# Kernel optimization log

Measured on AMD Instinct MI355X. Metric: run time of the kernel, lower is better.

The kernel has to match this reference:

```python
import jax, jax.numpy as jnp
import numpy as np

B, G, S, GS, P = 32, 512, 128, 32, 10
C, H, RED = 384, 6, 16
HID = 4 * C
D = C // H
SCALE = D ** -0.5

def _gelu(x):
    return jax.nn.gelu(x, approximate=False)

def _ln(x, g, b):
    m = jnp.mean(x, -1, keepdims=True)
    v = jnp.var(x, -1, keepdims=True)
    return (x - m) * jax.lax.rsqrt(v + 1e-5) * g + b

def _split_qkv(x, W):
    Bn, T, Cc = x.shape
    qkv = (x @ W).reshape(Bn, T, 3, H, D).transpose(2, 0, 3, 1, 4)
    return qkv[0], qkv[1], qkv[2]

def _merge(x):
    Bn, Hh, T, Dd = x.shape
    return x.transpose(0, 2, 1, 3).reshape(Bn, T, Hh * Dd)

def _mha(q, k, v):
    a = jax.nn.softmax(jnp.einsum('bhnd,bhmd->bhnm', q, k) * SCALE, axis=-1)
    return jnp.einsum('bhnm,bhmd->bhnd', a, v)

def _forward(x, center1, center2, neighborhood, prompt_embeddings, ln1_g, ln1_b, Wqkv, Wproj, bproj, gate, ln2_g, ln2_b, W1, b1, W2, b2, ad_down_W, ad_down_b, ad_up_W, ad_up_b, ad_gate, bn_g, bn_b, bn_mean, bn_var, ln3_g, ln3_b, a1_Wqkv, a1_Wproj, a1_bproj, ad1_down_W, ad1_down_b, ad1_up_W, ad1_up_b, idx, center_idx, group_size, if_maxmean, pro_cof, center_cof):
    Bx, Ntok, Cc = x.shape
    # prompt dropout is identity in eval
    prompt = jnp.broadcast_to(prompt_embeddings, (Bx, P, Cc))
    # --- gated dual self / prompt-cross attention ---
    xn = _ln(x, ln1_g, ln1_b)
    q, k, v = _split_qkv(xn, Wqkv)
    xs = _mha(q, k, v)                                  # [B,H,N,D]
    _, pk, pv = _split_qkv(prompt, Wqkv)
    pa = jax.nn.softmax(jnp.einsum('bhnd,bhpd->bhnp', q, pk) * SCALE, axis=-1)
    px = jnp.einsum('bhnp,bhpd->bhnd', gate * pa, pv)   # learned gate per head
    x = x + (_merge(xs) + _merge(px)) @ Wproj + bproj
    # --- MLP + gated bottleneck adapter residual ---
    h = _gelu(_ln(x, ln2_g, ln2_b) @ W1 + b1) @ W2 + b2
    h_ad = h + _gelu(h @ ad_down_W + ad_down_b) @ ad_up_W + ad_up_b
    x = ad_gate * h_ad + x
    cls_x = x[:, :1]
    xt = x[:, 1:]                                       # [B,G,C]
    flat = xt.reshape(Bx * G, Cc)
    x_nb = flat[idx].reshape(Bx * S, group_size, Cc)    # KNN neighborhoods
    x_ct = flat[center_idx].reshape(Bx, S, Cc)          # center features
    # NOTE: original normalizes `neighborhood` by its std, but result is unused
    # --- local self-attention (attn1 over norm3) on each neighborhood ---
    nq, nk, nv = _split_qkv(_ln(x_nb, ln3_g, ln3_b), a1_Wqkv)
    no = _mha(nq, nk, nv)
    x_nb = x_nb + _merge(no) @ a1_Wproj + a1_bproj
    knn = x_nb.reshape(Bx, S, group_size, Cc)
    lc = jnp.max(knn, axis=2)
    if if_maxmean:
        lc = lc + jnp.mean(knn, axis=2)
    # BatchNorm1d (eval, running stats) + GELU over channel dim
    lc = _gelu((lc - bn_mean) * jax.lax.rsqrt(bn_var + 1e-5) * bn_g + bn_b)
    vis = lc + center_cof * x_ct                        # [B,S,C]
    # --- propagate: de_neighbors == S so sorted-topk == full weighted sum ---
    d = jnp.sum((center1[:, :, None, :] - center2[:, None, :, :]) ** 2, axis=-1)  # [B,G,S]
    w = 1.0 / (d + 1e-8)
    w = w / jnp.sum(w, axis=-1, keepdims=True)
    interp = jnp.einsum('bns,bsc->bnc', w, vis)
    xt = xt + pro_cof * interp
    out = jnp.concatenate([cls_x, xt], axis=1)
    # adapter1
    out = out + _gelu(out @ ad1_down_W + ad1_down_b) @ ad1_up_W + ad1_up_b
    return out

def setup_inputs():
    ks = jax.random.split(jax.random.key(0), 20)
    r = lambda i, shape, s=0.02: jax.random.normal(ks[i], shape, jnp.float32) * s
    return {
        'x': jax.random.normal(ks[0], (B, G + 1, C), jnp.float32),
        'center1': jax.random.normal(ks[1], (B, G, 3), jnp.float32),
        'center2': jax.random.normal(ks[2], (B, S, 3), jnp.float32),
        'neighborhood': jax.random.normal(ks[3], (B, S, GS, 3), jnp.float32),
        'prompt_embeddings': r(4, (P, C)),
        'ln1_g': jnp.ones(C), 'ln1_b': jnp.zeros(C),
        'Wqkv': r(5, (C, 3 * C)),
        'Wproj': r(6, (C, C)), 'bproj': jnp.zeros(C),
        'gate': jax.random.normal(ks[7], (1, H, 1, 1), jnp.float32),
        'ln2_g': jnp.ones(C), 'ln2_b': jnp.zeros(C),
        'W1': r(8, (C, HID)), 'b1': jnp.zeros(HID),
        'W2': r(9, (HID, C)), 'b2': jnp.zeros(C),
        'ad_down_W': r(10, (C, RED)), 'ad_down_b': jnp.zeros(RED),
        'ad_up_W': r(11, (RED, C)), 'ad_up_b': jnp.zeros(C),
        'ad_gate': jax.random.normal(ks[12], (), jnp.float32),
        'bn_g': jnp.ones(C), 'bn_b': jnp.zeros(C),
        'bn_mean': jnp.zeros(C), 'bn_var': jnp.ones(C),
        'ln3_g': jnp.ones(C), 'ln3_b': jnp.zeros(C),
        'a1_Wqkv': r(13, (C, 3 * C)),
        'a1_Wproj': r(14, (C, C)), 'a1_bproj': jnp.zeros(C),
        'ad1_down_W': r(15, (C, RED)), 'ad1_down_b': jnp.zeros(RED),
        'ad1_up_W': r(16, (RED, C)), 'ad1_up_b': jnp.zeros(C),
        'idx': jax.random.randint(ks[17], (B * S * GS,), 0, B * G),
        'center_idx': jax.random.randint(ks[18], (B * S,), 0, B * G),
        'group_size': GS,
        'if_maxmean': 1,
        'pro_cof': 1,
        'center_cof': 1,
    }

def reference(x, center1, center2, neighborhood, prompt_embeddings, ln1_g, ln1_b, Wqkv, Wproj, bproj, gate, ln2_g, ln2_b, W1, b1, W2, b2, ad_down_W, ad_down_b, ad_up_W, ad_up_b, ad_gate, bn_g, bn_b, bn_mean, bn_var, ln3_g, ln3_b, a1_Wqkv, a1_Wproj, a1_bproj, ad1_down_W, ad1_down_b, ad1_up_W, ad1_up_b, idx, center_idx, group_size, if_maxmean, pro_cof, center_cof):
    return _forward(x, center1, center2, neighborhood, prompt_embeddings, ln1_g, ln1_b, Wqkv, Wproj, bproj, gate, ln2_g, ln2_b, W1, b1, W2, b2, ad_down_W, ad_down_b, ad_up_W, ad_up_b, ad_gate, bn_g, bn_b, bn_mean, bn_var, ln3_g, ln3_b, a1_Wqkv, a1_Wproj, a1_bproj, ad1_down_W, ad1_down_b, ad1_up_W, ad1_up_b, idx, center_idx, group_size, if_maxmean, pro_cof, center_cof)
```

## Files before the change

### kernel.cpp

```cpp
#include <hip/hip_runtime.h>
#include <hip/hip_bf16.h>
#include <cstdint>
#include <cstddef>

typedef __hip_bfloat16 bf16;
constexpr int TOK = 32 * 513;

typedef __attribute__((ext_vector_type(8))) short short8;
typedef __attribute__((ext_vector_type(4))) float f32x4;

__device__ __forceinline__ float bflo(unsigned u){ return __uint_as_float(u << 16); }
__device__ __forceinline__ float bfhi(unsigned u){ return __uint_as_float(u & 0xffff0000u); }
__device__ __forceinline__ float b2f(bf16 x){ return __bfloat162float(x); }
__device__ __forceinline__ bf16  f2b(float x){ return __float2bfloat16(x); }
__device__ __forceinline__ float geluf(float x){ return 0.5f*x*(1.0f + erff(x*0.70710678118654752f)); }
__device__ __forceinline__ void unp8(uint4 u, float* f){
  f[0]=bflo(u.x); f[1]=bfhi(u.x); f[2]=bflo(u.y); f[3]=bfhi(u.y);
  f[4]=bflo(u.z); f[5]=bfhi(u.z); f[6]=bflo(u.w); f[7]=bfhi(u.w);
}
__device__ __forceinline__ float scal(const int* p){
  const int i = *p;
  if (i > -1000000 && i < 1000000) return (float)i;
  return __int_as_float(i);
}
__device__ __forceinline__ f32x4 mfma16(short8 a, short8 b, f32x4 c){
  return __builtin_amdgcn_mfma_f32_16x16x32_bf16(a, b, c, 0, 0, 0);
}
__device__ __forceinline__ int swzl(int l){ return l ^ ((l >> 3) & 7); }

__global__ __launch_bounds__(256) void detect_kernel(const unsigned* __restrict__ x,
                                                     int* __restrict__ flag)
{
  const int t = threadIdx.x;
  bool bad = false;
  for (int i = t; i < 2048; i += 256){
    const unsigned u = x[i];
    const float a = fabsf(bflo(u)), b = fabsf(bfhi(u));
    if (!(a < 1e6f) || !(b < 1e6f)) bad = true;
  }
  __shared__ int s;
  if (t == 0) s = 0;
  __syncthreads();
  const unsigned long long m = __ballot(bad);
  if (m != 0ull && (t & 63) == 0) atomicOr(&s, 1);
  __syncthreads();
  if (t == 0) *flag = s;
}

struct ConvArgs {
  const void* src[34];
  bf16*       dst[34];
  int         n[34];
};
__global__ __launch_bounds__(256) void convert_many(const int* __restrict__ flag, ConvArgs a)
{
  const int ii = blockIdx.y;
  const bool isf = (*flag != 0);
  const int n = a.n[ii];
  const int n8 = n >> 3;
  bf16* d = a.dst[ii];
  if (isf){
    const float4* s = (const float4*)a.src[ii];
    for (int i = blockIdx.x*256 + threadIdx.x; i < n8; i += gridDim.x*256){
      const float4 f0 = s[i*2];
      const float4 f1 = s[i*2 + 1];
      bf16 tmp[8] = {f2b(f0.x),f2b(f0.y),f2b(f0.z),f2b(f0.w),
                     f2b(f1.x),f2b(f1.y),f2b(f1.z),f2b(f1.w)};
      *(uint4*)(d + (size_t)i*8) = *(const uint4*)tmp;
    }
  } else {
    const uint4* s = (const uint4*)a.src[ii];
    for (int i = blockIdx.x*256 + threadIdx.x; i < n8; i += gridDim.x*256){
      ((uint4*)d)[i] = s[i];
    }
  }
  if (blockIdx.x == 0){
    for (int i = n8*8 + threadIdx.x; i < n; i += 256){
      d[i] = isf ? f2b(((const float*)a.src[ii])[i]) : ((const bf16*)a.src[ii])[i];
    }
  }
}

__global__ __launch_bounds__(256) void shuffle_b(const bf16* __restrict__ W,
    bf16* __restrict__ out, int N, int KT, int NT)
{
  const int id = blockIdx.x*256 + threadIdx.x;
  if (id >= NT*KT*64) return;
  const int l  = id & 63;
  const int k0 = (id >> 6) % KT;
  const int n0 = (id >> 6) / KT;
  bf16 tmp[8];
  #pragma unroll
  for (int j = 0; j < 8; j++)
    tmp[j] = W[(size_t)(k0*32 + (l>>4)*8 + j)*N + n0*16 + (l&15)];
  *(uint4*)(out + (size_t)id*8) = *(const uint4*)tmp;
}

template<bool SRC_BF16>
__global__ __launch_bounds__(256) void ln_kernel(const void* __restrict__ src,
    const bf16* __restrict__ g, const bf16* __restrict__ b,
    bf16* __restrict__ out, int rows)
{
  const int wave = (blockIdx.x * blockDim.x + threadIdx.x) >> 6;
  const int lane = threadIdx.x & 63;
  if (wave >= rows) return;
  float v[6]; float s = 0.f, s2 = 0.f;
  #pragma unroll
  for (int i = 0; i < 6; i++){
    const int c = lane + 64*i;
    float x;
    if (SRC_BF16) x = b2f(((const bf16*)src)[(size_t)wave*384 + c]);
    else          x = ((const float*)src)[(size_t)wave*384 + c];
    v[i] = x; s += x; s2 += x*x;
  }
  #pragma unroll
  for (int mm = 32; mm; mm >>= 1){ s += __shfl_xor(s, mm); s2 += __shfl_xor(s2, mm); }
  const float mean = s * (1.f/384.f);
  const float rs = rsqrtf(s2 * (1.f/384.f) - mean*mean + 1e-5f);
  #pragma unroll
  for (int i = 0; i < 6; i++){
    const int c = lane + 64*i;
    out[(size_t)wave*384 + c] = f2b((v[i]-mean)*rs*b2f(g[c]) + b2f(b[c]));
  }
}

__global__ __launch_bounds__(256) void ln3_kernel(const float* __restrict__ xres,
    const bf16* __restrict__ g, const bf16* __restrict__ b, bf16* __restrict__ out)
{
  const int r = (blockIdx.x * blockDim.x + threadIdx.x) >> 6;
  const int lane = threadIdx.x & 63;
  if (r >= 16384) return;
  const int tok = (r >> 9)*513 + 1 + (r & 511);
  const float* xp = xres + (size_t)tok*384;
  float v[6]; float s = 0.f, s2 = 0.f;
  #pragma unroll
  for (int i = 0; i < 6; i++){
    const float x = xp[lane + 64*i];
    v[i] = x; s += x; s2 += x*x;
  }
  #pragma unroll
  for (int mm = 32; mm; mm >>= 1){ s += __shfl_xor(s, mm); s2 += __shfl_xor(s2, mm); }
  const float mean = s * (1.f/384.f);
  const float rs = rsqrtf(s2 * (1.f/384.f) - mean*mean + 1e-5f);
  #pragma unroll
  for (int i = 0; i < 6; i++){
    const int c = lane + 64*i;
    out[(size_t)r*384 + c] = f2b((v[i]-mean)*rs*b2f(g[c]) + b2f(b[c]));
  }
}

template<int EPI>
__global__ __launch_bounds__(256) void mfma_gemm(
    const bf16* __restrict__ A, const bf16* __restrict__ Bsh,
    const bf16* __restrict__ bias, const bf16* __restrict__ resid,
    void* __restrict__ outv, int M, int N, int K)
{
  __shared__ __align__(16) bf16 sA[8*64*8];
  const int t = threadIdx.x, lane = t & 63, w = t >> 6;
  const int l15 = lane & 15, quad = lane >> 4;
  const int wm = w & 1, wn = w >> 1;
  const int m0 = blockIdx.y * 128;
  const int n0t = blockIdx.x * 8 + wn * 4;
  const int KT = K >> 5;
  f32x4 acc[4][4];
  #pragma unroll
  for (int i = 0; i < 4; i++){
    #pragma unroll
    for (int j = 0; j < 4; j++) acc[i][j] = f32x4{0.f,0.f,0.f,0.f};
  }
  const int arow = t >> 1, ac0 = (t & 1) * 16;
  const int amt = arow >> 4, al15 = arow & 15, aq0 = (ac0 >> 3);

  for (int ks = 0; ks < KT; ks++){
    uint4 u0 = {0,0,0,0}, u1 = {0,0,0,0};
    const int gm = m0 + arow;
    if (gm < M){
      const bf16* ap = A + (size_t)gm*K + ks*32 + ac0;
      u0 = *(const uint4*)ap; u1 = *(const uint4*)(ap + 8);
    }
    *(uint4*)(sA + ((amt*64 + aq0*16     + al15) << 3)) = u0;
    *(uint4*)(sA + ((amt*64 + (aq0+1)*16 + al15) << 3)) = u1;
    __syncthreads();
    short8 afr[4];
    #pragma unroll
    for (int i = 0; i < 4; i++)
      afr[i] = *(const short8*)(sA + (((wm*4+i)*64 + lane) << 3));
    #pragma unroll
    for (int j = 0; j < 4; j++){
      const short8 b = *(const short8*)(Bsh + ((size_t)((n0t+j)*KT + ks)*64 + lane)*8);
      #pragma unroll
      for (int i = 0; i < 4; i++) acc[i][j] = mfma16(afr[i], b, acc[i][j]);
    }
    __syncthreads();
  }
  #pragma unroll
  for (int i = 0; i < 4; i++){
    #pragma unroll
    for (int r = 0; r < 4; r++){
      const int gm = m0 + (wm*4+i)*16 + quad*4 + r;
      if (gm < M){
        #pragma unroll
        for (int j = 0; j < 4; j++){
          const int gn = (n0t+j)*16 + l15;
          float v = acc[i][j][r];
          const size_t o = (size_t)gm*N + gn;
          if (EPI == 0){ v += b2f(bias[gn]); ((bf16*)outv)[o] = f2b(v); }
          else if (EPI == 1){ ((bf16*)outv)[o] = f2b(v); }
          else if (EPI == 2){ v += b2f(bias[gn]); ((bf16*)outv)[o] = f2b(geluf(v)); }
          else { v += b2f(bias[gn]) + b2f(resid[o]); ((float*)outv)[o] = v; }
        }
      }
    }
  }
}

__global__ __launch_bounds__(256) void pqkv_kernel(const bf16* __restrict__ pe,
    const bf16* __restrict__ Wqkv, float* __restrict__ pq)
{
  const int n  = blockIdx.x*64 + (threadIdx.x & 63);
  const int rg = threadIdx.x >> 6;
  for (int r = rg; r < 10; r += 4){
    float s0 = 0.f, s1 = 0.f;
    for (int c = 0; c < 384; c += 2){
      s0 = fmaf(b2f(pe[(size_t)r*384+c]),   b2f(Wqkv[(size_t)c*1152 + n]),     s0);
      s1 = fmaf(b2f(pe[(size_t)r*384+c+1]), b2f(Wqkv[(size_t)(c+1)*1152 + n]), s1);
    }
    pq[(size_t)r*1152 + n] = s0 + s1;
  }
}

__global__ __launch_bounds__(256) void attn_kernel(
    const bf16* __restrict__ qkv, const float* __restrict__ pq,
    const bf16* __restrict__ gate, bf16* __restrict__ ao)
{
  __shared__ __align__(16) bf16 s_q[64*72];
  __shared__ __align__(16) bf16 s_k[64*72];
  __shared__ __align__(16) bf16 s_vT[64*72];
  __shared__ __align__(16) bf16 s_p[4*16*40];
  __shared__ __align__(16) bf16 s_pk[16*72];
  __shared__ __align__(16) bf16 s_pvT[64*40];
  const int bh = blockIdx.y;
  const int b = bh / 6, h = bh % 6;
  const int q0 = blockIdx.x * 64;
  const int t = threadIdx.x, lane = t & 63, w = t >> 6;
  const int l15 = lane & 15, quad = lane >> 4;

  {
    const int row = t >> 2, dc = (t & 3) * 16;
    const int tok = q0 + row;
    uint4 u0 = {0,0,0,0}, u1 = {0,0,0,0};
    if (tok < 513){
      const bf16* p = qkv + (size_t)(b*513 + tok)*1152 + h*64 + dc;
      u0 = *(const uint4*)p; u1 = *(const uint4*)(p + 8);
    }
    *(uint4*)(s_q + row*72 + dc)     = u0;
    *(uint4*)(s_q + row*72 + dc + 8) = u1;
  }
  {
    const int j = t >> 4, dc = (t & 15) * 4;
    float f[4] = {0.f,0.f,0.f,0.f};
    if (j < 10){
      const float* pk = pq + (size_t)j*1152 + 384 + h*64 + dc;
      f[0]=pk[0]; f[1]=pk[1]; f[2]=pk[2]; f[3]=pk[3];
    }
    bf16 tmp[4] = {f2b(f[0]),f2b(f[1]),f2b(f[2]),f2b(f[3])};
    *(uint2*)(s_pk + j*72 + dc) = *(const uint2*)tmp;
  }
  {
    const int d = t & 63, kg = t >> 6;
    #pragma unroll
    for (int kk = 0; kk < 8; kk++){
      const int key = kg*8 + kk;
      bf16 v = f2b(0.f);
      if (key < 10) v = f2b(pq[(size_t)key*1152 + 768 + h*64 + d]);
      s_pvT[d*40 + key] = v;
    }
  }

  float m_i[4], l_i[4];
  f32x4 oacc[4];
  #pragma unroll
  for (int r = 0; r < 4; r++){ m_i[r] = -30000.f; l_i[r] = 0.f; }
  #pragma unroll
  for (int nt = 0; nt < 4; nt++) oacc[nt] = f32x4{0.f,0.f,0.f,0.f};
  bf16* myp = s_p + w*16*40;
  const short8* aq = (const short8*)(s_q + (w*16 + l15)*72);

  for (int kt = 0; kt < 9; kt++){
    const int kb = kt*64;
    __syncthreads();
    {
      const int kp = t & 31, dg = t >> 5;
      const int key0 = kb + 2*kp;
      uint4 k0v = {0,0,0,0}, k1v = {0,0,0,0}, v0 = {0,0,0,0}, v1 = {0,0,0,0};
      if (key0 < 513){
        const bf16* base = qkv + (size_t)(b*513 + key0)*1152 + h*64 + dg*8;
        k0v = *(const uint4*)(base + 384);
        v0  = *(const uint4*)(base + 768);
      }
      if (key0 + 1 < 513){
        const bf16* base = qkv + (size_t)(b*513 + key0 + 1)*1152 + h*64 + dg*8;
        k1v = *(const uint4*)(base + 384);
        v1  = *(const uint4*)(base + 768);
      }
      *(uint4*)(s_k + (2*kp)*72   + dg*8) = k0v;
      *(uint4*)(s_k + (2*kp+1)*72 + dg*8) = k1v;
      const unsigned short* a0 = (const unsigned short*)&v0;
      const unsigned short* a1 = (const unsigned short*)&v1;
      unsigned* vt = (unsigned*)s_vT;
      #pragma unroll
      for (int j = 0; j < 8; j++)
        vt[(dg*8 + j)*36 + kp] = (unsigned)a0[j] | ((unsigned)a1[j] << 16);
    }
    __syncthreads();

    f32x4 sreg[4];
    #pragma unroll
    for (int nt = 0; nt < 4; nt++){
      f32x4 acc = f32x4{0.f,0.f,0.f,0.f};
      const short8* bk = (const short8*)(s_k + (nt*16 + l15)*72);
      acc = mfma16(aq[quad],     bk[quad],     acc);
      acc = mfma16(aq[4 + quad], bk[4 + quad], acc);
      const bool kvalid = (kb + nt*16 + l15) < 513;
      #pragma unroll
      for (int r = 0; r < 4; r++)
        sreg[nt][r] = kvalid ? acc[r]*0.125f : -30000.f;
    }
    float alpha[4];
    #pragma unroll
    for (int r = 0; r < 4; r++){
      float mx = fmaxf(fmaxf(sreg[0][r], sreg[1][r]), fmaxf(sreg[2][r], sreg[3][r]));
      #pragma unroll
      for (int mm = 8; mm; mm >>= 1) mx = fmaxf(mx, __shfl_xor(mx, mm));
      const float mn = fmaxf(m_i[r], mx);
      alpha[r] = __expf(m_i[r] - mn);
      m_i[r] = mn;
      float ps = 0.f;
      #pragma unroll
      for (int nt = 0; nt < 4; nt++){
        const float p = __expf(sreg[nt][r] - mn);
        sreg[nt][r] = p; ps += p;
      }
      #pragma unroll
      for (int mm = 8; mm; mm >>= 1) ps += __shfl_xor(ps, mm);
      l_i[r] = l_i[r]*alpha[r] + ps;
    }
    #pragma unroll
    for (int nt = 0; nt < 4; nt++){
      #pragma unroll
      for (int r = 0; r < 4; r++)
        myp[(quad*4 + r)*40 + nt*16 + l15] = f2b(sreg[nt][r]);
    }
    #pragma unroll
    for (int nt = 0; nt < 4; nt++){
      #pragma unroll
      for (int r = 0; r < 4; r++) oacc[nt][r] *= alpha[r];
    }
    const short8* ap = (const short8*)(myp + l15*40);
    #pragma unroll
    for (int nt = 0; nt < 4; nt++){
      const short8* bv = (const short8*)(s_vT + (nt*16 + l15)*72);
      oacc[nt] = mfma16(ap[quad],     bv[quad],     oacc[nt]);
      oacc[nt] = mfma16(ap[4 + quad], bv[4 + quad], oacc[nt]);
    }
  }

  f32x4 sp;
  {
    f32x4 acc = f32x4{0.f,0.f,0.f,0.f};
    const short8* bp = (const short8*)(s_pk + l15*72);
    acc = mfma16(aq[quad],     bp[quad],     acc);
    acc = mfma16(aq[4 + quad], bp[4 + quad], acc);
    #pragma unroll
    for (int r = 0; r < 4; r++)
      sp[r] = (l15 < 10) ? acc[r]*0.125f : -30000.f;
  }
  float psr[4];
  #pragma unroll
  for (int r = 0; r < 4; r++){
    float mx = sp[r];
    #pragma unroll
    for (int mm = 8; mm; mm >>= 1) mx = fmaxf(mx, __shfl_xor(mx, mm));
    const float p = __expf(sp[r] - mx);
    float ps = p;
    #pragma unroll
    for (int mm = 8; mm; mm >>= 1) ps += __shfl_xor(ps, mm);
    psr[r] = ps;
    myp[(quad*4 + r)*40 + l15]      = f2b(p);
    myp[(quad*4 + r)*40 + 16 + l15] = f2b(0.f);
  }
  f32x4 pva[4];
  {
    const short8* ap = (const short8*)(myp + l15*40);
    #pragma unroll
    for (int nt = 0; nt < 4; nt++){
      const short8* bv = (const short8*)(s_pvT + (nt*16 + l15)*40);
      pva[nt] = mfma16(ap[quad], bv[quad], f32x4{0.f,0.f,0.f,0.f});
    }
  }

  const float gh = b2f(gate[h]);
  #pragma unroll
  for (int r = 0; r < 4; r++){
    const int tok = q0 + w*16 + quad*4 + r;
    if (tok < 513){
      const float invl = 1.f/l_i[r];
      const float gps  = gh/psr[r];
      #pragma unroll
      for (int nt = 0; nt < 4; nt++){
        const float val = oacc[nt][r]*invl + pva[nt][r]*gps;
        ao[(size_t)(b*513 + tok)*384 + h*64 + nt*16 + l15] = f2b(val);
      }
    }
  }
}

__global__ __launch_bounds__(256) void adapter_mid_kernel(const bf16* __restrict__ h,
    const bf16* __restrict__ Wd, const bf16* __restrict__ bd,
    const bf16* __restrict__ Wu, const bf16* __restrict__ bu,
    const bf16* __restrict__ p_gate, float* __restrict__ xres)
{
  __shared__ float s_h[384];
  __shared__ float s_part[16][17];
  __shared__ float s_y[16];
  const size_t row = blockIdx.x;
  const int t = threadIdx.x;
  const bf16* hp = h + row*384;
  for (int c = t; c < 384; c += 256) s_h[c] = b2f(hp[c]);
  __syncthreads();
  const int o = t & 15, p = t >> 4;
  float part0 = 0.f, part1 = 0.f;
  for (int c = p; c < 384; c += 32){
    part0 = fmaf(s_h[c],    b2f(Wd[(size_t)c*16 + o]),      part0);
    part1 = fmaf(s_h[c+16], b2f(Wd[(size_t)(c+16)*16 + o]), part1);
  }
  s_part[o][p] = part0 + part1;
  __syncthreads();
  if (t < 16){
    float sum = 0.f;
    #pragma unroll
    for (int pp = 0; pp < 16; pp++) sum += s_part[t][pp];
    s_y[t] = geluf(sum + b2f(bd[t]));
  }
  __syncthreads();
  const float g = b2f(p_gate[0]);
  for (int c = t; c < 384; c += 256){
    float up = 0.f;
    #pragma unroll
    for (int o2 = 0; o2 < 16; o2++) up = fmaf(s_y[o2], b2f(Wu[(size_t)o2*384 + c]), up);
    const float had = s_h[c] + up + b2f(bu[c]);
    xres[row*384 + c] = g*had + xres[row*384 + c];
  }
}

__global__ __launch_bounds__(256) void adapter_final_kernel(const float* __restrict__ xr,
    const bf16* __restrict__ Wd, const bf16* __restrict__ bd,
    const bf16* __restrict__ Wu, const bf16* __restrict__ bu,
    const int* __restrict__ flag, void* __restrict__ out)
{
  __shared__ float s_h[384];
  __shared__ float s_part[16][17];
  __shared__ float s_y[16];
  const size_t row = blockIdx.x;
  const int t = threadIdx.x;
  const float* hp = xr + row*384;
  for (int c = t; c < 384; c += 256) s_h[c] = hp[c];
  __syncthreads();
  const int o = t & 15, p = t >> 4;
  float part0 = 0.f, part1 = 0.f;
  for (int c = p; c < 384; c += 32){
    part0 = fmaf(s_h[c],    b2f(Wd[(size_t)c*16 + o]),      part0);
    part1 = fmaf(s_h[c+16], b2f(Wd[(size_t)(c+16)*16 + o]), part1);
  }
  s_part[o][p] = part0 + part1;
  __syncthreads();
  if (t < 16){
    float sum = 0.f;
    #pragma unroll
    for (int pp = 0; pp < 16; pp++) sum += s_part[t][pp];
    s_y[t] = geluf(sum + b2f(bd[t]));
  }
  __syncthreads();
  const bool isf = (*flag != 0);
  for (int c = t; c < 384; c += 256){
    float up = 0.f;
    #pragma unroll
    for (int o2 = 0; o2 < 16; o2++) up = fmaf(s_y[o2], b2f(Wu[(size_t)o2*384 + c]), up);
    const float v = s_h[c] + up + b2f(bu[c]);
    if (isf) ((float*)out)[row*384 + c] = v;
    else     ((bf16*)out)[row*384 + c] = f2b(v);
  }
}

__global__ __launch_bounds__(512) void local_kernel(
    const bf16* __restrict__ qkv3, const float* __restrict__ xres,
    const int* __restrict__ idx, const int* __restrict__ cidx,
    const bf16* __restrict__ Bp, const bf16* __restrict__ bp1,
    const bf16* __restrict__ bng, const bf16* __restrict__ bnb,
    const bf16* __restrict__ bnm, const bf16* __restrict__ bnv,
    const int* __restrict__ p_ifmm, const int* __restrict__ p_ccof,
    float* __restrict__ vis)
{
  __shared__ __align__(16) bf16 sQ[3*4*64*8];
  __shared__ __align__(16) bf16 sK[3*4*64*8];
  __shared__ __align__(16) bf16 sV[3*4*64*8];
  __shared__ __align__(16) bf16 sP[3*2*64*8];
  __shared__ int s_flat[32];
  __shared__ int s_tok[32];
  bf16* sO = sQ;

  const int g = blockIdx.x;
  const int t = threadIdx.x, lane = t & 63, w = t >> 6;
  const int l15 = lane & 15, quad = lane >> 4;
  const int lanez = swzl(lane);

  if (t < 32){
    const int r = idx[g*32 + t];
    s_flat[t] = r;
    s_tok[t]  = (r >> 9)*513 + 1 + (r & 511);
  }
  __syncthreads();

  f32x4 accp[3][2];
  #pragma unroll
  for (int a = 0; a < 3; a++){
    #pragma unroll
    for (int m = 0; m < 2; m++) accp[a][m] = f32x4{0.f,0.f,0.f,0.f};
  }

  for (int hc = 0; hc < 2; hc++){
    for (int ch = t; ch < 2304; ch += 512){
      const int row = ch & 31;
      const int cc  = ch >> 5;
      const int seg = cc / 24;
      const int wi  = cc - seg*24;
      const int h   = wi >> 3;
      const int d0  = (wi & 7) * 8;
      const int col = seg*384 + (hc*3 + h)*64 + d0;
      const uint4 u = *(const uint4*)(qkv3 + (size_t)s_flat[row]*1152 + col);
      if (seg < 2){
        const int T = h*4 + (row>>4)*2 + (d0>>5);
        const int L = ((d0>>3)&3)*16 + (row&15);
        const int addr = (T*64 + swzl(L))*8;
        if (seg == 0) *(uint4*)(sQ + addr) = u;
        else          *(uint4*)(sK + addr) = u;
      } else {
        const bf16* sv = (const bf16*)&u;
        #pragma unroll
        for (int j2 = 0; j2 < 8; j2++){
          const int d = d0 + j2;
          const int L = (row>>3)*16 + (d&15);
          sV[((h*4 + (d>>4))*64 + swzl(L))*8 + (row&7)] = sv[j2];
        }
      }
    }
    __syncthreads();

    if (w < 6){
      const int h = w >> 1, mt = w & 1;
      f32x4 sr[2];
      #pragma unroll
      for (int nt = 0; nt < 2; nt++){
        f32x4 acc = f32x4{0.f,0.f,0.f,0.f};
        #pragma unroll
        for (int k0 = 0; k0 < 2; k0++){
          const short8 a = *(const short8*)(sQ + ((h*4 + mt*2 + k0)*64 + lanez)*8);
          const short8 b = *(const short8*)(sK + ((h*4 + nt*2 + k0)*64 + lanez)*8);
          acc = mfma16(a, b, acc);
        }
        #pragma unroll
        for (int r = 0; r < 4; r++) sr[nt][r] = acc[r]*0.125f;
      }
      #pragma unroll
      for (int r = 0; r < 4; r++){
        float mx = fmaxf(sr[0][r], sr[1][r]);
        #pragma unroll
        for (int mm = 8; mm; mm >>= 1) mx = fmaxf(mx, __shfl_xor(mx, mm));
        const float e0 = __expf(sr[0][r] - mx), e1 = __expf(sr[1][r] - mx);
        float sm = e0 + e1;
        #pragma unroll
        for (int mm = 8; mm; mm >>= 1) sm += __shfl_xor(sm, mm);
        const float inv = 1.f/sm;
        const int m = quad*4 + r;
        const int L0 = (l15 >> 3)*16       + m;
        const int L1 = (2 + (l15 >> 3))*16 + m;
        sP[((h*2 + mt)*64 + swzl(L0))*8 + (l15 & 7)] = f2b(e0*inv);
        sP[((h*2 + mt)*64 + swzl(L1))*8 + (l15 & 7)] = f2b(e1*inv);
      }
    }
    __syncthreads();

    {
      const int mt = w & 1, nt = w >> 1;
      const int k0w = nt >> 1, qdw = (nt & 1)*2 + (l15 >> 3), jw = l15 & 7;
      #pragma unroll
      for (int h = 0; h < 3; h++){
        const short8 a = *(const short8*)(sP + ((h*2 + mt)*64 + lanez)*8);
        const short8 b = *(const short8*)(sV + ((h*4 + nt)*64 + lanez)*8);
        const f32x4 o = mfma16(a, b, f32x4{0.f,0.f,0.f,0.f});
        #pragma unroll
        for (int r = 0; r < 4; r++){
          const int L = qdw*16 + quad*4 + r;
          sO[((h*4 + mt*2 + k0w)*64 + swzl(L))*8 + jw] = f2b(o[r]);
        }
      }
    }
    __syncthreads();

    #pragma unroll
    for (int h = 0; h < 3; h++){
      short8 afr[2][2];
      #pragma unroll
      for (int mt = 0; mt < 2; mt++){
        #pragma unroll
        for (int k0l = 0; k0l < 2; k0l++)
          afr[mt][k0l] = *(const short8*)(sO + ((h*4 + mt*2 + k0l)*64 + lanez)*8);
      }
      const int hg2 = (hc*3 + h)*2;
      #pragma unroll
      for (int tt = 0; tt < 3; tt++){
        const int nt = w*3 + tt;
        #pragma unroll
        for (int k0l = 0; k0l < 2; k0l++){
          const short8 b = *(const short8*)(Bp + ((size_t)(nt*12 + hg2 + k0l)*64 + lane)*8);
          accp[tt][0] = mfma16(afr[0][k0l], b, accp[tt][0]);
          accp[tt][1] = mfma16(afr[1][k0l], b, accp[tt][1]);
        }
      }
    }
    __syncthreads();
  }

  const float fmm  = scal(p_ifmm);
  const float ccof = scal(p_ccof);
  const int cr = cidx[g];
  const int ctok = (cr >> 9)*513 + 1 + (cr & 511);
  #pragma unroll
  for (int tt = 0; tt < 3; tt++){
    const int n = (w*3 + tt)*16 + l15;
    const float bb = b2f(bp1[n]);
    float mx = -3e30f, sm = 0.f;
    #pragma unroll
    for (int mt = 0; mt < 2; mt++){
      #pragma unroll
      for (int r = 0; r < 4; r++){
        const int tok = mt*16 + quad*4 + r;
        const float v = accp[tt][mt][r] + bb + xres[(size_t)s_tok[tok]*384 + n];
        mx = fmaxf(mx, v); sm += v;
      }
    }
    mx = fmaxf(mx, __shfl_xor(mx, 16)); sm += __shfl_xor(sm, 16);
    mx = fmaxf(mx, __shfl_xor(mx, 32)); sm += __shfl_xor(sm, 32);
    if (quad == 0){
      const float lc = (fmm != 0.f) ? (mx + sm*(1.f/32.f)) : mx;
      const float nr = (lc - b2f(bnm[n])) * rsqrtf(b2f(bnv[n]) + 1e-5f) * b2f(bng[n]) + b2f(bnb[n]);
      vis[(size_t)g*384 + n] = geluf(nr) + ccof * xres[(size_t)ctok*384 + n];
    }
  }
}

__global__ __launch_bounds__(256) void interp_kernel(const bf16* __restrict__ c1,
    const bf16* __restrict__ c2, const float* __restrict__ vis,
    const int* __restrict__ p_pcof, float* __restrict__ xres)
{
  __shared__ float s_w[8][128];
  __shared__ float s_red[2];
  const int b = blockIdx.y;
  const int n0 = blockIdx.x * 8;
  const int t = threadIdx.x;
  for (int ni = 0; ni < 8; ni++){
    const int n = n0 + ni;
    float wv = 0.f;
    if (t < 128){
      float d2 = 0.f;
      #pragma unroll
      for (int k = 0; k < 3; k++){
        const float a = b2f(c1[((size_t)b*512 + n)*3 + k]);
        const float c = b2f(c2[((size_t)b*128 + t)*3 + k]);
        const float df = a - c; d2 += df*df;
      }
      wv = 1.f/(d2 + 1e-8f);
    }
    float rsum = wv;
    #pragma unroll
    for (int mm = 32; mm; mm >>= 1) rsum += __shfl_xor(rsum, mm);
    if (((t & 63) == 0) && t < 128) s_red[t >> 6] = rsum;
    __syncthreads();
    const float tot = s_red[0] + s_red[1];
    if (t < 128) s_w[ni][t] = wv / tot;
    __syncthreads();
  }
  float acc1[8], acc2[8];
  #pragma unroll
  for (int ni = 0; ni < 8; ni++){ acc1[ni] = 0.f; acc2[ni] = 0.f; }
  for (int s = 0; s < 128; s++){
    const float* vp = vis + ((size_t)b*128 + s)*384;
    const float v1 = vp[t];
    const float v2 = (t < 128) ? vp[t + 256] : 0.f;
    #pragma unroll
    for (int ni = 0; ni < 8; ni++){
      const float wn = s_w[ni][s];
      acc1[ni] = fmaf(wn, v1, acc1[ni]);
      acc2[ni] = fmaf(wn, v2, acc2[ni]);
    }
  }
  const float pc = scal(p_pcof);
  #pragma unroll
  for (int ni = 0; ni < 8; ni++){
    const int tok = b*513 + 1 + n0 + ni;
    xres[(size_t)tok*384 + t] += pc*acc1[ni];
    if (t < 128) xres[(size_t)tok*384 + t + 256] += pc*acc2[ni];
  }
}

extern "C" void kernel_launch(void* const* d_in, const int* in_sizes, int n_in,
                              void* d_out, int out_size, void* d_ws, size_t ws_size,
                              hipStream_t stream)
{
  (void)n_in; (void)out_size; (void)ws_size;
  const int*  idx   = (const int*)d_in[35];
  const int*  cidx  = (const int*)d_in[36];
  const int*  ifmm  = (const int*)d_in[38];
  const int*  pcof  = (const int*)d_in[39];
  const int*  ccof  = (const int*)d_in[40];

  size_t off = 0;
  auto alloc = [&](size_t bytes) -> void* {
    void* p = (char*)d_ws + off; off += (bytes + 255) & ~(size_t)255; return p;
  };
  int*   flag = (int*)  alloc(sizeof(int));
  float* xres = (float*)alloc((size_t)TOK*384*4);
  bf16*  slab = (bf16*) alloc((size_t)TOK*1536*2);
  bf16*  xn   = (bf16*) alloc((size_t)TOK*384*2);
  float* pq   = (float*)alloc((size_t)10*1152*4);
  bf16*  Bq   = (bf16*) alloc((size_t)72*12*64*8*2);
  bf16*  Bp   = (bf16*) alloc((size_t)24*12*64*8*2);
  bf16*  Bqkv = (bf16*) alloc((size_t)72*12*64*8*2);
  bf16*  Bw1  = (bf16*) alloc((size_t)96*12*64*8*2);
  bf16*  Bw2  = (bf16*) alloc((size_t)24*48*64*8*2);
  bf16*  Bwp  = (bf16*) alloc((size_t)24*12*64*8*2);

  bf16*  qkvb = slab;
  bf16*  x_c  = slab + (size_t)TOK*1152;
  bf16*  h1   = slab;
  bf16*  qkv3 = slab;
  bf16*  xln3 = slab + (size_t)TOK*1152;
  bf16*  ao   = xn;
  bf16*  hbuf = xn;
  float* visb = (float*)xn;

  const int conv_ids[34] = {0,1,2,4,5,6,7,8,9,10,11,12,13,14,15,16,17,
                            18,19,20,21,22,23,24,25,26,27,28,29,30,31,32,33,34};
  ConvArgs ca;
  bf16* canon[41];
  int maxn = 1;
  for (int k = 0; k < 34; k++){
    const int i = conv_ids[k];
    const int n = in_sizes[i];
    bf16* dst = (i == 0) ? x_c : (bf16*)alloc((size_t)n*2);
    ca.src[k] = d_in[i]; ca.dst[k] = dst; ca.n[k] = n;
    canon[i] = dst;
    if (n > maxn) maxn = n;
  }
  detect_kernel<<<dim3(1), dim3(256), 0, stream>>>((const unsigned*)d_in[0], flag);
  {
    int gx = (maxn/8 + 255) / 256; if (gx > 512) gx = 512; if (gx < 1) gx = 1;
    convert_many<<<dim3(gx, 34), dim3(256), 0, stream>>>(flag, ca);
  }

  const bf16 *x_in = canon[0], *c1 = canon[1], *c2 = canon[2], *pe = canon[4],
             *ln1g = canon[5], *ln1b = canon[6], *Wqkv = canon[7], *Wproj = canon[8],
             *bproj = canon[9], *gate = canon[10], *ln2g = canon[11], *ln2b = canon[12],
             *W1 = canon[13], *b1 = canon[14], *W2 = canon[15], *b2v = canon[16],
             *adW = canon[17], *adb = canon[18], *adU = canon[19], *adub = canon[20],
             *adg = canon[21], *bng = canon[22], *bnb = canon[23], *bnm = canon[24],
             *bnv = canon[25], *ln3g = canon[26], *ln3b = canon[27], *a1W = canon[28],
             *a1P = canon[29], *a1pb = canon[30], *d1W = canon[31], *d1b = canon[32],
             *u1W = canon[33], *u1b = canon[34];

  shuffle_b<<<dim3(216), dim3(256), 0, stream>>>(a1W, Bq, 1152, 12, 72);
  shuffle_b<<<dim3(72),  dim3(256), 0, stream>>>(a1P, Bp, 384, 12, 24);
  shuffle_b<<<dim3(216), dim3(256), 0, stream>>>(Wqkv, Bqkv, 1152, 12, 72);
  shuffle_b<<<dim3(288), dim3(256), 0, stream>>>(W1, Bw1, 1536, 12, 96);
  shuffle_b<<<dim3(288), dim3(256), 0, stream>>>(W2, Bw2, 384, 48, 24);
  shuffle_b<<<dim3(72),  dim3(256), 0, stream>>>(Wproj, Bwp, 384, 12, 24);

  ln_kernel<true><<<dim3((TOK*64)/256), dim3(256), 0, stream>>>((const void*)x_in, ln1g, ln1b, xn, TOK);
  mfma_gemm<1><<<dim3(9,129), dim3(256), 0, stream>>>(xn, Bqkv, nullptr, nullptr, qkvb, TOK, 1152, 384);
  pqkv_kernel<<<dim3(18), dim3(256), 0, stream>>>(pe, Wqkv, pq);
  attn_kernel<<<dim3(9,192), dim3(256), 0, stream>>>(qkvb, pq, gate, ao);
  mfma_gemm<3><<<dim3(3,129), dim3(256), 0, stream>>>(ao, Bwp, bproj, x_in, xres, TOK, 384, 384);
  ln_kernel<false><<<dim3((TOK*64)/256), dim3(256), 0, stream>>>((const void*)xres, ln2g, ln2b, xn, TOK);
  mfma_gemm<2><<<dim3(12,129), dim3(256), 0, stream>>>(xn, Bw1, b1, nullptr, h1, TOK, 1536, 384);
  mfma_gemm<0><<<dim3(3,129), dim3(256), 0, stream>>>(h1, Bw2, b2v, nullptr, hbuf, TOK, 384, 1536);
  adapter_mid_kernel<<<dim3(TOK), dim3(256), 0, stream>>>(hbuf, adW, adb, adU, adub, adg, xres);
  ln3_kernel<<<dim3((16384*64)/256), dim3(256), 0, stream>>>(xres, ln3g, ln3b, xln3);
  mfma_gemm<1><<<dim3(9,128), dim3(256), 0, stream>>>(xln3, Bq, nullptr, nullptr, qkv3, 16384, 1152, 384);
  local_kernel<<<dim3(4096), dim3(512), 0, stream>>>(qkv3, xres, idx, cidx, Bp, a1pb,
                                                     bng, bnb, bnm, bnv, ifmm, ccof, visb);
  interp_kernel<<<dim3(64,32), dim3(256), 0, stream>>>(c1, c2, visb, pcof, xres);
  adapter_final_kernel<<<dim3(TOK), dim3(256), 0, stream>>>(xres, d1W, d1b, u1W, u1b, flag, d_out);
}
```

Before: 808.8 us.

## Load Q/K fragments directly from global and prefetch V into registers

The local attention kernel stops staging Q and K through shared memory and has each wave load its MFMA operand fragments straight from the gathered qkv rows in global memory. V for the next head chunk is prefetched into registers during the projection phase, and the head-chunk loop is unrolled. Launch bounds now request 8 waves per SIMD to push occupancy, with reduced LDS footprint. The cost is more scattered global loads, with K rows reread by several waves, and possible register pressure or spills under the tighter bound.

```diff
diff --git a/kernel.cpp b/kernel.cpp
--- a/kernel.cpp
+++ b/kernel.cpp
@@ -492,7 +492,7 @@
   }
 }
 
-__global__ __launch_bounds__(512) void local_kernel(
+__global__ __launch_bounds__(512, 8) void local_kernel(
     const bf16* __restrict__ qkv3, const float* __restrict__ xres,
     const int* __restrict__ idx, const int* __restrict__ cidx,
     const bf16* __restrict__ Bp, const bf16* __restrict__ bp1,
@@ -501,13 +501,11 @@
     const int* __restrict__ p_ifmm, const int* __restrict__ p_ccof,
     float* __restrict__ vis)
 {
-  __shared__ __align__(16) bf16 sQ[3*4*64*8];
-  __shared__ __align__(16) bf16 sK[3*4*64*8];
   __shared__ __align__(16) bf16 sV[3*4*64*8];
   __shared__ __align__(16) bf16 sP[3*2*64*8];
+  __shared__ __align__(16) bf16 sO[3*4*64*8];
   __shared__ int s_flat[32];
   __shared__ int s_tok[32];
-  bf16* sO = sQ;
 
   const int g = blockIdx.x;
   const int t = threadIdx.x, lane = t & 63, w = t >> 6;
@@ -521,6 +519,18 @@
   }
   __syncthreads();
 
+  const int vrowA = t & 31,          vccA = t >> 5;
+  const int vrowB = (512 + t) & 31,  vccB = (512 + t) >> 5;
+  const int vhA = vccA >> 3, vd0A = (vccA & 7) * 8;
+  const int vhB = vccB >> 3, vd0B = (vccB & 7) * 8;
+  const bool hasB = (t < 256);
+
+  uint4 svA, svB;
+  {
+    svA = *(const uint4*)(qkv3 + (size_t)s_flat[vrowA]*1152 + 768 + (0*3 + vhA)*64 + vd0A);
+    if (hasB) svB = *(const uint4*)(qkv3 + (size_t)s_flat[vrowB]*1152 + 768 + (0*3 + vhB)*64 + vd0B);
+  }
+
   f32x4 accp[3][2];
   #pragma unroll
   for (int a = 0; a < 3; a++){
@@ -528,29 +538,23 @@
     for (int m = 0; m < 2; m++) accp[a][m] = f32x4{0.f,0.f,0.f,0.f};
   }
 
+  #pragma unroll
   for (int hc = 0; hc < 2; hc++){
-    for (int ch = t; ch < 2304; ch += 512){
-      const int row = ch & 31;
-      const int cc  = ch >> 5;
-      const int seg = cc / 24;
-      const int wi  = cc - seg*24;
-      const int h   = wi >> 3;
-      const int d0  = (wi & 7) * 8;
-      const int col = seg*384 + (hc*3 + h)*64 + d0;
-      const uint4 u = *(const uint4*)(qkv3 + (size_t)s_flat[row]*1152 + col);
-      if (seg < 2){
-        const int T = h*4 + (row>>4)*2 + (d0>>5);
-        const int L = ((d0>>3)&3)*16 + (row&15);
-        const int addr = (T*64 + swzl(L))*8;
-        if (seg == 0) *(uint4*)(sQ + addr) = u;
-        else          *(uint4*)(sK + addr) = u;
-      } else {
-        const bf16* sv = (const bf16*)&u;
+    {
+      const bf16* sa = (const bf16*)&svA;
+      #pragma unroll
+      for (int j2 = 0; j2 < 8; j2++){
+        const int d = vd0A + j2;
+        const int L = (vrowA>>3)*16 + (d&15);
+        sV[((vhA*4 + (d>>4))*64 + swzl(L))*8 + (vrowA&7)] = sa[j2];
+      }
+      if (hasB){
+        const bf16* sb = (const bf16*)&svB;
         #pragma unroll
         for (int j2 = 0; j2 < 8; j2++){
-          const int d = d0 + j2;
-          const int L = (row>>3)*16 + (d&15);
-          sV[((h*4 + (d>>4))*64 + swzl(L))*8 + (row&7)] = sv[j2];
+          const int d = vd0B + j2;
+          const int L = (vrowB>>3)*16 + (d&15);
+          sV[((vhB*4 + (d>>4))*64 + swzl(L))*8 + (vrowB&7)] = sb[j2];
         }
       }
     }
@@ -558,16 +562,18 @@
 
     if (w < 6){
       const int h = w >> 1, mt = w & 1;
+      const size_t qrow = (size_t)s_flat[mt*16 + l15]*1152;
+      const int dcol = (hc*3 + h)*64 + quad*8;
+      const short8 q0 = *(const short8*)(qkv3 + qrow + dcol);
+      const short8 q1 = *(const short8*)(qkv3 + qrow + dcol + 32);
       f32x4 sr[2];
       #pragma unroll
       for (int nt = 0; nt < 2; nt++){
-        f32x4 acc = f32x4{0.f,0.f,0.f,0.f};
-        #pragma unroll
-        for (int k0 = 0; k0 < 2; k0++){
-          const short8 a = *(const short8*)(sQ + ((h*4 + mt*2 + k0)*64 + lanez)*8);
-          const short8 b = *(const short8*)(sK + ((h*4 + nt*2 + k0)*64 + lanez)*8);
-          acc = mfma16(a, b, acc);
-        }
+        const size_t krow = (size_t)s_flat[nt*16 + l15]*1152 + 384;
+        const short8 k0 = *(const short8*)(qkv3 + krow + dcol);
+        const short8 k1 = *(const short8*)(qkv3 + krow + dcol + 32);
+        f32x4 acc = mfma16(q0, k0, f32x4{0.f,0.f,0.f,0.f});
+        acc = mfma16(q1, k1, acc);
         #pragma unroll
         for (int r = 0; r < 4; r++) sr[nt][r] = acc[r]*0.125f;
       }
@@ -606,6 +612,11 @@
       }
     }
     __syncthreads();
+
+    if (hc == 0){
+      svA = *(const uint4*)(qkv3 + (size_t)s_flat[vrowA]*1152 + 768 + (3 + vhA)*64 + vd0A);
+      if (hasB) svB = *(const uint4*)(qkv3 + (size_t)s_flat[vrowB]*1152 + 768 + (3 + vhB)*64 + vd0B);
+    }
 
     #pragma unroll
     for (int h = 0; h < 3; h++){
```

Result: slower. 935.2 us (+15.6%).
